# Performance work log

Measured on AMD Instinct MI355X. Metric: run time of the kernel, lower is better.

Reference implementation:

```python
import jax, jax.numpy as jnp
import numpy as np

B, S, H, E, K = 4, 2048, 2048, 8, 2


def setup_inputs() -> dict:
    key = jax.random.key(0)
    k1, k2, k3 = jax.random.split(key, 3)
    scale = 1.0 / np.sqrt(H)
    return {
        "x": jax.random.normal(k1, (B, S, H), dtype=jnp.float32),
        "Wg": jax.random.normal(k2, (H, E), dtype=jnp.float32) * scale,
        "bg": jnp.zeros((E,), dtype=jnp.float32),
        "W": jax.random.normal(k3, (E, H, H), dtype=jnp.float32) * scale,
        "b": jnp.zeros((E, H), dtype=jnp.float32),
        "topk": K,
    }


def reference(x, Wg, bg, W, b, topk):
    Bsz, Sl, Hd = x.shape
    n_exp = W.shape[0]
    hs = x.reshape(-1, Hd)                              # [T, H] flattened tokens
    # Router: linear gate -> softmax -> top-k -> renormalize
    router_logits = hs @ Wg + bg                        # [T, E]
    probs = jax.nn.softmax(router_logits, axis=-1)
    top_w, sel = jax.lax.top_k(probs, topk)             # [T, K]
    top_w = top_w / jnp.sum(top_w, axis=-1, keepdims=True)
    # Per-token combine coefficient for each expert (sums weights over top-k slots)
    coef = jnp.einsum("tk,tke->te", top_w,
                      jax.nn.one_hot(sel, n_exp, dtype=hs.dtype))  # [T, E]
    # Dense grouped expert MLP: y_e = hs @ W_e + b_e, then weighted combine.
    h = jnp.einsum("th,ehf->etf", hs, W) + b[:, None, :]  # [E, T, H]
    out = jnp.einsum("te,etf->tf", coef, h)               # [T, H]
    return out.reshape(Bsz, Sl, Hd), router_logits
```

## Files before the change

### kernel.cpp

```cpp
#include <hip/hip_runtime.h>
#include <math.h>

#define T_TOK 8192
#define HD    2048
#define NE    8
#define BM    128
#define BN    128
#define NT    (HD / 64)
#define MAXT  136
#define RMAX  17408

typedef __bf16 bf16x4 __attribute__((ext_vector_type(4)));
typedef __bf16 bf16x8 __attribute__((ext_vector_type(8)));
typedef float  f32x4  __attribute__((ext_vector_type(4)));

#define GLOAD16(src, dst)                                                              \
    __builtin_amdgcn_global_load_lds((__attribute__((address_space(1))) void*)(src),   \
                                     (__attribute__((address_space(3))) void*)(dst),   \
                                     16, 0, 0)

__global__ __launch_bounds__(256) void router_cvt_kernel(
    const float* __restrict__ x, const float* __restrict__ Wg,
    const float* __restrict__ bg, float* __restrict__ logits_out,
    int* __restrict__ tok_exp, float* __restrict__ tok_w,
    __bf16* __restrict__ xb, int* __restrict__ cnt)
{
    __shared__ int hbin[NE];
    const int lane = threadIdx.x & 63;
    const int wv   = threadIdx.x >> 6;
    const int t    = blockIdx.x * 4 + wv;
    const float* xr  = x  + (size_t)t * HD;
    __bf16*      xbr = xb + (size_t)t * HD;

    if (threadIdx.x < NE) hbin[threadIdx.x] = 0;
    __syncthreads();

    float acc[8] = {0.f,0.f,0.f,0.f,0.f,0.f,0.f,0.f};
#pragma unroll
    for (int j = 0; j < 8; ++j) {
        const int h0 = j * 256 + lane * 4;
        float4 xv = *reinterpret_cast<const float4*>(xr + h0);
        bf16x4 bv;
        bv[0] = (__bf16)xv.x; bv[1] = (__bf16)xv.y;
        bv[2] = (__bf16)xv.z; bv[3] = (__bf16)xv.w;
        *reinterpret_cast<bf16x4*>(xbr + h0) = bv;

        const float4* wg = reinterpret_cast<const float4*>(Wg + (size_t)h0 * NE);
        float xs[4] = {xv.x, xv.y, xv.z, xv.w};
#pragma unroll
        for (int r = 0; r < 4; ++r) {
            float4 wa = wg[r * 2], wb = wg[r * 2 + 1];
            acc[0] += xs[r] * wa.x; acc[1] += xs[r] * wa.y;
            acc[2] += xs[r] * wa.z; acc[3] += xs[r] * wa.w;
            acc[4] += xs[r] * wb.x; acc[5] += xs[r] * wb.y;
            acc[6] += xs[r] * wb.z; acc[7] += xs[r] * wb.w;
        }
    }
#pragma unroll
    for (int off = 32; off; off >>= 1) {
#pragma unroll
        for (int e = 0; e < 8; ++e) acc[e] += __shfl_xor(acc[e], off);
    }
    if (lane == 0) {
        float lg[8];
#pragma unroll
        for (int e = 0; e < 8; ++e) lg[e] = acc[e] + bg[e];
        float4* lo = reinterpret_cast<float4*>(logits_out + (size_t)t * NE);
        lo[0] = make_float4(lg[0], lg[1], lg[2], lg[3]);
        lo[1] = make_float4(lg[4], lg[5], lg[6], lg[7]);
        int i0 = 0;
        for (int e = 1; e < 8; ++e) if (lg[e] > lg[i0]) i0 = e;
        int i1 = (i0 == 0) ? 1 : 0;
        for (int e = 0; e < 8; ++e) if (e != i0 && lg[e] > lg[i1]) i1 = e;
        float d = expf(lg[i1] - lg[i0]);
        float inv = 1.0f / (1.0f + d);
        tok_exp[t * 2]     = i0;
        tok_exp[t * 2 + 1] = i1;
        tok_w[t * 2]       = inv;
        tok_w[t * 2 + 1]   = d * inv;
        atomicAdd(&hbin[i0], 1);
        atomicAdd(&hbin[i1], 1);
    }
    __syncthreads();
    if (threadIdx.x < NE && hbin[threadIdx.x] > 0)
        atomicAdd(&cnt[threadIdx.x], hbin[threadIdx.x]);
}

__global__ __launch_bounds__(256) void wt_kernel(const float* __restrict__ W,
                                                 __bf16* __restrict__ Wt)
{
    const int e  = blockIdx.z;
    const int k0 = blockIdx.y * 64;
    const int f0 = blockIdx.x * 64;
    __shared__ float T[64][65];

    const int t  = threadIdx.x;
    const int fi = (t & 15) * 4;
    const int kb = t >> 4;
    const float* src = W + (size_t)e * HD * HD + (size_t)(k0 + kb) * HD + f0 + fi;
#pragma unroll
    for (int j = 0; j < 4; ++j) {
        float4 v = *reinterpret_cast<const float4*>(src + (size_t)j * 16 * HD);
        int k = kb + j * 16;
        T[k][fi + 0] = v.x;
        T[k][fi + 1] = v.y;
        T[k][fi + 2] = v.z;
        T[k][fi + 3] = v.w;
    }
    __syncthreads();
    const int f  = t >> 2;
    const int kc = (t & 3) * 16;
    bf16x8 o0, o1;
#pragma unroll
    for (int j = 0; j < 8; ++j) o0[j] = (__bf16)T[kc + j][f];
#pragma unroll
    for (int j = 0; j < 8; ++j) o1[j] = (__bf16)T[kc + 8 + j][f];
    __bf16* dst = Wt + (size_t)e * HD * HD + (size_t)(f0 + f) * HD + k0 + kc;
    *reinterpret_cast<bf16x8*>(dst)     = o0;
    *reinterpret_cast<bf16x8*>(dst + 8) = o1;
}

__global__ void scan_kernel(const int* __restrict__ cnt, int* __restrict__ cursor,
                            int* __restrict__ tile_exp, int* __restrict__ tile_row0,
                            int* __restrict__ ntiles)
{
    if (threadIdx.x == 0) {
        int off = 0, nt = 0;
        for (int e = 0; e < NE; ++e) {
            cursor[e] = off;
            int c = cnt[e];
            int tiles = (c + 127) >> 7;
            for (int i = 0; i < tiles; ++i) {
                tile_exp[nt]  = e;
                tile_row0[nt] = off + (i << 7);
                ++nt;
            }
            off += tiles << 7;
        }
        *ntiles = nt;
    }
}

__global__ __launch_bounds__(256) void scatter_kernel(
    const int* __restrict__ tok_exp, const float* __restrict__ tok_w,
    int* __restrict__ cursor, int* __restrict__ row_token, float* __restrict__ row_coef)
{
    __shared__ int lcnt[NE];
    __shared__ int lbase[NE];
    const int tid = threadIdx.x;
    if (tid < NE) lcnt[tid] = 0;
    __syncthreads();
    const int s = blockIdx.x * 256 + tid;
    const int e = tok_exp[s];
    const int r = atomicAdd(&lcnt[e], 1);
    __syncthreads();
    if (tid < NE) lbase[tid] = atomicAdd(&cursor[tid], lcnt[tid]);
    __syncthreads();
    const int pos = lbase[e] + r;
    row_token[pos] = s >> 1;
    row_coef[pos]  = tok_w[s];
}

__global__ __launch_bounds__(256, 2) void moe_gemm_128(
    const __bf16* __restrict__ xb, const __bf16* __restrict__ Wt,
    const float* __restrict__ bexp,
    const int* __restrict__ tile_exp, const int* __restrict__ tile_row0,
    const int* __restrict__ ntiles_p, const int* __restrict__ row_token,
    const float* __restrict__ row_coef, float* __restrict__ out)
{
    const int rt = blockIdx.y;
    if (rt >= *ntiles_p) return;
    const int e  = tile_exp[rt];
    const int r0 = tile_row0[rt];
    const int cb = blockIdx.x * BN;

    __shared__ __align__(16) char lds[65536];

    const int tid  = threadIdx.x;
    const int lane = tid & 63;
    const int wv   = tid >> 6;
    const int wr   = (wv >> 1) * 64;
    const int wc   = (wv & 1) * 64;

    const int colS = ((((tid & 7) * 16) ^ (((tid >> 3) & 7) << 4))) >> 1;

    const __bf16* srcA[4];
    const __bf16* srcB[4];
#pragma unroll
    for (int i = 0; i < 4; ++i) {
        int gr  = i * 32 + (tid >> 3);
        int tok = row_token[r0 + gr];
        if (tok < 0) tok = 0;
        srcA[i] = xb + (size_t)tok * HD + colS;
        srcB[i] = Wt + ((size_t)e << 22) + (size_t)(cb + gr) * HD + colS;
    }

    f32x4 acc[4][4];
#pragma unroll
    for (int m = 0; m < 4; ++m)
#pragma unroll
        for (int n = 0; n < 4; ++n) acc[m][n] = (f32x4){0.f, 0.f, 0.f, 0.f};

    const int fr    = lane & 15;
    const int swz   = (lane & 7) << 4;
    const int koff0 = (((lane >> 4) * 16)      ) ^ swz;
    const int koff1 = (((lane >> 4) * 16) + 64 ) ^ swz;

    {
        char* d0 = lds + wv * 1024;
        char* d1 = d0 + 32768;
#pragma unroll
        for (int i = 0; i < 4; ++i) GLOAD16(srcA[i], d0 + i * 4096);
#pragma unroll
        for (int i = 0; i < 4; ++i) GLOAD16(srcB[i], d0 + 16384 + i * 4096);
#pragma unroll
        for (int i = 0; i < 4; ++i) GLOAD16(srcA[i] + 64, d1 + i * 4096);
#pragma unroll
        for (int i = 0; i < 4; ++i) GLOAD16(srcB[i] + 64, d1 + 16384 + i * 4096);
    }

#pragma unroll 2
    for (int t = 0; t < NT; ++t) {
        if (t < NT - 1) { asm volatile("s_waitcnt vmcnt(8)" ::: "memory"); }
        else            { asm volatile("s_waitcnt vmcnt(0)" ::: "memory"); }
        __builtin_amdgcn_s_barrier();

        const char* ab = lds + (t & 1) * 32768;
        const char* bb = ab + 16384;

        bf16x8 bfr0[4], bfr1[4];
#pragma unroll
        for (int n = 0; n < 4; ++n) {
            int rowb = (wc + n * 16 + fr) << 7;
            bfr0[n] = *reinterpret_cast<const bf16x8*>(bb + (rowb + koff0));
            bfr1[n] = *reinterpret_cast<const bf16x8*>(bb + (rowb + koff1));
        }
        __builtin_amdgcn_s_setprio(1);
#pragma unroll
        for (int m = 0; m < 4; ++m) {
            int rowa = (wr + m * 16 + fr) << 7;
            bf16x8 a0 = *reinterpret_cast<const bf16x8*>(ab + (rowa + koff0));
            bf16x8 a1 = *reinterpret_cast<const bf16x8*>(ab + (rowa + koff1));
#pragma unroll
            for (int n = 0; n < 4; ++n) {
                acc[m][n] = __builtin_amdgcn_mfma_f32_16x16x32_bf16(a0, bfr0[n], acc[m][n], 0, 0, 0);
                acc[m][n] = __builtin_amdgcn_mfma_f32_16x16x32_bf16(a1, bfr1[n], acc[m][n], 0, 0, 0);
            }
        }
        __builtin_amdgcn_s_setprio(0);

        if (t < NT - 2) {
            asm volatile("s_waitcnt lgkmcnt(0)" ::: "memory");
            __builtin_amdgcn_s_barrier();
            const int nk = (t + 2) * 64;
            char* dA = lds + (t & 1) * 32768 + wv * 1024;
#pragma unroll
            for (int i = 0; i < 4; ++i) GLOAD16(srcA[i] + nk, dA + i * 4096);
#pragma unroll
            for (int i = 0; i < 4; ++i) GLOAD16(srcB[i] + nk, dA + 16384 + i * 4096);
        }
    }

    const int rj = (lane >> 4) * 4;
    float bias_[4];
#pragma unroll
    for (int n = 0; n < 4; ++n)
        bias_[n] = bexp[(size_t)e * HD + cb + wc + n * 16 + fr];

#pragma unroll
    for (int m = 0; m < 4; ++m) {
        const int lr = wr + m * 16 + rj;
        int tok[4]; float cf[4];
#pragma unroll
        for (int j = 0; j < 4; ++j) {
            tok[j] = row_token[r0 + lr + j];
            cf[j]  = row_coef[r0 + lr + j];
        }
#pragma unroll
        for (int n = 0; n < 4; ++n) {
            const int f = cb + wc + n * 16 + fr;
#pragma unroll
            for (int j = 0; j < 4; ++j) {
                if (tok[j] >= 0)
                    atomicAdd(&out[(size_t)tok[j] * HD + f], (acc[m][n][j] + bias_[n]) * cf[j]);
            }
        }
    }
}

extern "C" void kernel_launch(void* const* d_in, const int* in_sizes, int n_in,
                              void* d_out, int out_size, void* d_ws, size_t ws_size,
                              hipStream_t stream)
{
    (void)in_sizes; (void)n_in; (void)out_size; (void)ws_size;

    const float* x  = (const float*)d_in[0];
    const float* Wg = (const float*)d_in[1];
    const float* bg = (const float*)d_in[2];
    const float* W  = (const float*)d_in[3];
    const float* b  = (const float*)d_in[4];

    float* out    = (float*)d_out;
    float* logits = out + (size_t)T_TOK * HD;

    char* p = (char*)d_ws;
    int*   cnt       = (int*)p;   p += NE * 4;
    int*   cursor    = (int*)p;   p += NE * 4;
    int*   ntiles    = (int*)p;   p += 8;
    int*   tile_exp  = (int*)p;   p += MAXT * 4;
    int*   tile_row0 = (int*)p;   p += MAXT * 4;
    int*   tok_exp   = (int*)p;   p += T_TOK * 2 * 4;
    float* tok_w     = (float*)p; p += T_TOK * 2 * 4;
    int*   row_token = (int*)p;   p += RMAX * 4;
    float* row_coef  = (float*)p; p += RMAX * 4;
    p = (char*)(((size_t)p + 255) & ~(size_t)255);
    __bf16* xb = (__bf16*)p;      p += (size_t)T_TOK * HD * 2;
    __bf16* Wt = (__bf16*)p;      p += (size_t)NE * HD * HD * 2;

    hipMemsetAsync(cnt, 0, NE * 4, stream);
    hipMemsetAsync(row_token, 0xFF, RMAX * 4, stream);
    hipMemsetAsync(out, 0, (size_t)T_TOK * HD * sizeof(float), stream);

    router_cvt_kernel<<<T_TOK / 4, 256, 0, stream>>>(x, Wg, bg, logits,
                                                     tok_exp, tok_w, xb, cnt);
    wt_kernel<<<dim3(HD / 64, HD / 64, NE), 256, 0, stream>>>(W, Wt);
    scan_kernel<<<1, 64, 0, stream>>>(cnt, cursor, tile_exp, tile_row0, ntiles);
    scatter_kernel<<<T_TOK * 2 / 256, 256, 0, stream>>>(tok_exp, tok_w, cursor,
                                                        row_token, row_coef);

    dim3 grid(HD / BN, MAXT);
    moe_gemm_128<<<grid, 256, 0, stream>>>(xb, Wt, b, tile_exp, tile_row0, ntiles,
                                           row_token, row_coef, out);
}
```

Before: 334.2 us.

## Halve GEMM K-tile to 32 to cut LDS and target four blocks per CU

Shrinks the per-stage K slice of the grouped expert GEMM from 64 to 32. This halves LDS use to 32 KB and raises launch bounds to 4 blocks per CU, with a new swizzled LDS layout that packs two rows per 128-byte line. The aim is more occupancy to hide global-load latency. The cost is twice as many barriers and waitcnt steps per K, and tighter register limits that could cause spills with 64 accumulators per thread.

```diff
diff --git a/kernel.cpp b/kernel.cpp
--- a/kernel.cpp
+++ b/kernel.cpp
@@ -6,7 +6,7 @@
 #define NE    8
 #define BM    128
 #define BN    128
-#define NT    (HD / 64)
+#define NT2   (HD / 32)
 #define MAXT  136
 #define RMAX  17408
 
@@ -161,7 +161,7 @@
     row_coef[pos]  = tok_w[s];
 }
 
-__global__ __launch_bounds__(256, 2) void moe_gemm_128(
+__global__ __launch_bounds__(256, 4) void moe_gemm_128(
     const __bf16* __restrict__ xb, const __bf16* __restrict__ Wt,
     const float* __restrict__ bexp,
     const int* __restrict__ tile_exp, const int* __restrict__ tile_row0,
@@ -174,7 +174,7 @@
     const int r0 = tile_row0[rt];
     const int cb = blockIdx.x * BN;
 
-    __shared__ __align__(16) char lds[65536];
+    __shared__ __align__(16) char lds[32768];
 
     const int tid  = threadIdx.x;
     const int lane = tid & 63;
@@ -182,17 +182,19 @@
     const int wr   = (wv >> 1) * 64;
     const int wc   = (wv & 1) * 64;
 
-    const int colS = ((((tid & 7) * 16) ^ (((tid >> 3) & 7) << 4))) >> 1;
-
-    const __bf16* srcA[4];
-    const __bf16* srcB[4];
-#pragma unroll
-    for (int i = 0; i < 4; ++i) {
-        int gr  = i * 32 + (tid >> 3);
+    const int c2      = (tid & 7) ^ ((tid >> 3) & 7);
+    const int kcolS   = (c2 & 3) * 8;
+    const int rowbase = ((tid >> 3) << 1) + (c2 >> 2);
+
+    const __bf16* srcA[2];
+    const __bf16* srcB[2];
+#pragma unroll
+    for (int i = 0; i < 2; ++i) {
+        int gr  = i * 64 + rowbase;
         int tok = row_token[r0 + gr];
         if (tok < 0) tok = 0;
-        srcA[i] = xb + (size_t)tok * HD + colS;
-        srcB[i] = Wt + ((size_t)e << 22) + (size_t)(cb + gr) * HD + colS;
+        srcA[i] = xb + (size_t)tok * HD + kcolS;
+        srcB[i] = Wt + ((size_t)e << 22) + (size_t)(cb + gr) * HD + kcolS;
     }
 
     f32x4 acc[4][4];
@@ -201,63 +203,59 @@
 #pragma unroll
         for (int n = 0; n < 4; ++n) acc[m][n] = (f32x4){0.f, 0.f, 0.f, 0.f};
 
-    const int fr    = lane & 15;
-    const int swz   = (lane & 7) << 4;
-    const int koff0 = (((lane >> 4) * 16)      ) ^ swz;
-    const int koff1 = (((lane >> 4) * 16) + 64 ) ^ swz;
+    const int fr = lane & 15;
+    const int kb = lane >> 4;
+
+    auto lds_off = [&](int row) -> int {
+        int r2 = row >> 1;
+        return r2 * 128 + (((((row & 1) << 2) + kb) ^ (r2 & 7)) << 4);
+    };
 
     {
         char* d0 = lds + wv * 1024;
-        char* d1 = d0 + 32768;
-#pragma unroll
-        for (int i = 0; i < 4; ++i) GLOAD16(srcA[i], d0 + i * 4096);
-#pragma unroll
-        for (int i = 0; i < 4; ++i) GLOAD16(srcB[i], d0 + 16384 + i * 4096);
-#pragma unroll
-        for (int i = 0; i < 4; ++i) GLOAD16(srcA[i] + 64, d1 + i * 4096);
-#pragma unroll
-        for (int i = 0; i < 4; ++i) GLOAD16(srcB[i] + 64, d1 + 16384 + i * 4096);
+        char* d1 = d0 + 16384;
+#pragma unroll
+        for (int i = 0; i < 2; ++i) GLOAD16(srcA[i],      d0 + i * 4096);
+#pragma unroll
+        for (int i = 0; i < 2; ++i) GLOAD16(srcB[i],      d0 + 8192 + i * 4096);
+#pragma unroll
+        for (int i = 0; i < 2; ++i) GLOAD16(srcA[i] + 32, d1 + i * 4096);
+#pragma unroll
+        for (int i = 0; i < 2; ++i) GLOAD16(srcB[i] + 32, d1 + 8192 + i * 4096);
     }
 
 #pragma unroll 2
-    for (int t = 0; t < NT; ++t) {
-        if (t < NT - 1) { asm volatile("s_waitcnt vmcnt(8)" ::: "memory"); }
-        else            { asm volatile("s_waitcnt vmcnt(0)" ::: "memory"); }
+    for (int t = 0; t < NT2; ++t) {
+        if (t < NT2 - 1) { asm volatile("s_waitcnt vmcnt(4)" ::: "memory"); }
+        else             { asm volatile("s_waitcnt vmcnt(0)" ::: "memory"); }
         __builtin_amdgcn_s_barrier();
 
-        const char* ab = lds + (t & 1) * 32768;
-        const char* bb = ab + 16384;
-
-        bf16x8 bfr0[4], bfr1[4];
-#pragma unroll
-        for (int n = 0; n < 4; ++n) {
-            int rowb = (wc + n * 16 + fr) << 7;
-            bfr0[n] = *reinterpret_cast<const bf16x8*>(bb + (rowb + koff0));
-            bfr1[n] = *reinterpret_cast<const bf16x8*>(bb + (rowb + koff1));
-        }
+        const char* ab = lds + (t & 1) * 16384;
+        const char* bb = ab + 8192;
+
+        bf16x8 bfr[4];
+#pragma unroll
+        for (int n = 0; n < 4; ++n)
+            bfr[n] = *reinterpret_cast<const bf16x8*>(bb + lds_off(wc + n * 16 + fr));
         __builtin_amdgcn_s_setprio(1);
 #pragma unroll
         for (int m = 0; m < 4; ++m) {
-            int rowa = (wr + m * 16 + fr) << 7;
-            bf16x8 a0 = *reinterpret_cast<const bf16x8*>(ab + (rowa + koff0));
-            bf16x8 a1 = *reinterpret_cast<const bf16x8*>(ab + (rowa + koff1));
-#pragma unroll
-            for (int n = 0; n < 4; ++n) {
-                acc[m][n] = __builtin_amdgcn_mfma_f32_16x16x32_bf16(a0, bfr0[n], acc[m][n], 0, 0, 0);
-                acc[m][n] = __builtin_amdgcn_mfma_f32_16x16x32_bf16(a1, bfr1[n], acc[m][n], 0, 0, 0);
-            }
+            bf16x8 a0 = *reinterpret_cast<const bf16x8*>(ab + lds_off(wr + m * 16 + fr));
+#pragma unroll
+            for (int n = 0; n < 4; ++n)
+                acc[m][n] = __builtin_amdgcn_mfma_f32_16x16x32_bf16(a0, bfr[n], acc[m][n], 0, 0, 0);
         }
         __builtin_amdgcn_s_setprio(0);
 
-        if (t < NT - 2) {
+        if (t < NT2 - 2) {
             asm volatile("s_waitcnt lgkmcnt(0)" ::: "memory");
             __builtin_amdgcn_s_barrier();
-            const int nk = (t + 2) * 64;
-            char* dA = lds + (t & 1) * 32768 + wv * 1024;
-#pragma unroll
-            for (int i = 0; i < 4; ++i) GLOAD16(srcA[i] + nk, dA + i * 4096);
-#pragma unroll
-            for (int i = 0; i < 4; ++i) GLOAD16(srcB[i] + nk, dA + 16384 + i * 4096);
+            const int nk = (t + 2) * 32;
+            char* dA = lds + (t & 1) * 16384 + wv * 1024;
+#pragma unroll
+            for (int i = 0; i < 2; ++i) GLOAD16(srcA[i] + nk, dA + i * 4096);
+#pragma unroll
+            for (int i = 0; i < 2; ++i) GLOAD16(srcB[i] + nk, dA + 8192 + i * 4096);
         }
     }
 
```

New measurement: 367.7 us. 10.0% more time.

## Pre-pack expert weights in MFMA fragment order and load B directly to registers

Applied to the files above, without the earlier changes.

The weight transpose kernel now writes each expert matrix in a layout where each lane's MFMA B fragment is a contiguous 16-byte chunk. The GEMM loads B straight from global memory into double-buffered registers instead of staging it through LDS. This halves the LDS footprint so the launch bound asks for three blocks per CU. The trade is more vector registers, and each B fragment is now read from global/L2 by every wave that uses it instead of once per block through shared memory.

```diff
diff --git a/kernel.cpp b/kernel.cpp
--- a/kernel.cpp
+++ b/kernel.cpp
@@ -18,6 +18,8 @@
     __builtin_amdgcn_global_load_lds((__attribute__((address_space(1))) void*)(src),   \
                                      (__attribute__((address_space(3))) void*)(dst),   \
                                      16, 0, 0)
+
+#define MEMFENCE() asm volatile("" ::: "memory")
 
 __global__ __launch_bounds__(256) void router_cvt_kernel(
     const float* __restrict__ x, const float* __restrict__ Wg,
@@ -86,8 +88,8 @@
         atomicAdd(&cnt[threadIdx.x], hbin[threadIdx.x]);
 }
 
-__global__ __launch_bounds__(256) void wt_kernel(const float* __restrict__ W,
-                                                 __bf16* __restrict__ Wt)
+__global__ __launch_bounds__(256) void wt2_kernel(const float* __restrict__ W,
+                                                  __bf16* __restrict__ Wt2)
 {
     const int e  = blockIdx.z;
     const int k0 = blockIdx.y * 64;
@@ -109,15 +111,24 @@
     }
     __syncthreads();
     const int f  = t >> 2;
-    const int kc = (t & 3) * 16;
+    const int c0 = (t & 3) * 2;
+    const int kc = c0 * 8;
     bf16x8 o0, o1;
 #pragma unroll
     for (int j = 0; j < 8; ++j) o0[j] = (__bf16)T[kc + j][f];
 #pragma unroll
     for (int j = 0; j < 8; ++j) o1[j] = (__bf16)T[kc + 8 + j][f];
-    __bf16* dst = Wt + (size_t)e * HD * HD + (size_t)(f0 + f) * HD + k0 + kc;
-    *reinterpret_cast<bf16x8*>(dst)     = o0;
-    *reinterpret_cast<bf16x8*>(dst + 8) = o1;
+
+    const int fb = (f0 >> 4) + (f >> 4);
+#pragma unroll
+    for (int j = 0; j < 2; ++j) {
+        const int ch   = c0 + j;
+        const int kbo  = (k0 >> 5) + (ch >> 2);
+        const int lane = (f & 15) + ((ch & 3) << 4);
+        size_t off = ((size_t)e << 22) + ((size_t)fb << 15) + ((size_t)kbo << 9)
+                   + ((size_t)lane << 3);
+        *reinterpret_cast<bf16x8*>(Wt2 + off) = (j == 0) ? o0 : o1;
+    }
 }
 
 __global__ void scan_kernel(const int* __restrict__ cnt, int* __restrict__ cursor,
@@ -161,8 +172,8 @@
     row_coef[pos]  = tok_w[s];
 }
 
-__global__ __launch_bounds__(256, 2) void moe_gemm_128(
-    const __bf16* __restrict__ xb, const __bf16* __restrict__ Wt,
+__global__ __launch_bounds__(256, 3) void moe_gemm_128(
+    const __bf16* __restrict__ xb, const __bf16* __restrict__ Wt2,
     const float* __restrict__ bexp,
     const int* __restrict__ tile_exp, const int* __restrict__ tile_row0,
     const int* __restrict__ ntiles_p, const int* __restrict__ row_token,
@@ -174,7 +185,7 @@
     const int r0 = tile_row0[rt];
     const int cb = blockIdx.x * BN;
 
-    __shared__ __align__(16) char lds[65536];
+    __shared__ __align__(16) char lds[32768];
 
     const int tid  = threadIdx.x;
     const int lane = tid & 63;
@@ -185,15 +196,16 @@
     const int colS = ((((tid & 7) * 16) ^ (((tid >> 3) & 7) << 4))) >> 1;
 
     const __bf16* srcA[4];
-    const __bf16* srcB[4];
 #pragma unroll
     for (int i = 0; i < 4; ++i) {
         int gr  = i * 32 + (tid >> 3);
         int tok = row_token[r0 + gr];
         if (tok < 0) tok = 0;
         srcA[i] = xb + (size_t)tok * HD + colS;
-        srcB[i] = Wt + ((size_t)e << 22) + (size_t)(cb + gr) * HD + colS;
-    }
+    }
+
+    const __bf16* bptr = Wt2 + ((size_t)e << 22)
+                       + ((size_t)((cb + wc) >> 4) << 15) + ((size_t)lane << 3);
 
     f32x4 acc[4][4];
 #pragma unroll
@@ -206,60 +218,77 @@
     const int koff0 = (((lane >> 4) * 16)      ) ^ swz;
     const int koff1 = (((lane >> 4) * 16) + 64 ) ^ swz;
 
+    bf16x8 breg[2][4][2];
+
     {
         char* d0 = lds + wv * 1024;
-        char* d1 = d0 + 32768;
+        char* d1 = d0 + 16384;
 #pragma unroll
         for (int i = 0; i < 4; ++i) GLOAD16(srcA[i], d0 + i * 4096);
-#pragma unroll
-        for (int i = 0; i < 4; ++i) GLOAD16(srcB[i], d0 + 16384 + i * 4096);
+        MEMFENCE();
+#pragma unroll
+        for (int n = 0; n < 4; ++n)
+#pragma unroll
+            for (int ks = 0; ks < 2; ++ks)
+                breg[0][n][ks] = *reinterpret_cast<const bf16x8*>(
+                    bptr + ((size_t)n << 15) + ((size_t)ks << 9));
+        MEMFENCE();
 #pragma unroll
         for (int i = 0; i < 4; ++i) GLOAD16(srcA[i] + 64, d1 + i * 4096);
-#pragma unroll
-        for (int i = 0; i < 4; ++i) GLOAD16(srcB[i] + 64, d1 + 16384 + i * 4096);
-    }
-
-#pragma unroll 2
-    for (int t = 0; t < NT; ++t) {
-        if (t < NT - 1) { asm volatile("s_waitcnt vmcnt(8)" ::: "memory"); }
-        else            { asm volatile("s_waitcnt vmcnt(0)" ::: "memory"); }
-        __builtin_amdgcn_s_barrier();
-
-        const char* ab = lds + (t & 1) * 32768;
-        const char* bb = ab + 16384;
-
-        bf16x8 bfr0[4], bfr1[4];
-#pragma unroll
-        for (int n = 0; n < 4; ++n) {
-            int rowb = (wc + n * 16 + fr) << 7;
-            bfr0[n] = *reinterpret_cast<const bf16x8*>(bb + (rowb + koff0));
-            bfr1[n] = *reinterpret_cast<const bf16x8*>(bb + (rowb + koff1));
-        }
-        __builtin_amdgcn_s_setprio(1);
-#pragma unroll
-        for (int m = 0; m < 4; ++m) {
-            int rowa = (wr + m * 16 + fr) << 7;
-            bf16x8 a0 = *reinterpret_cast<const bf16x8*>(ab + (rowa + koff0));
-            bf16x8 a1 = *reinterpret_cast<const bf16x8*>(ab + (rowa + koff1));
-#pragma unroll
-            for (int n = 0; n < 4; ++n) {
-                acc[m][n] = __builtin_amdgcn_mfma_f32_16x16x32_bf16(a0, bfr0[n], acc[m][n], 0, 0, 0);
-                acc[m][n] = __builtin_amdgcn_mfma_f32_16x16x32_bf16(a1, bfr1[n], acc[m][n], 0, 0, 0);
-            }
-        }
-        __builtin_amdgcn_s_setprio(0);
-
-        if (t < NT - 2) {
-            asm volatile("s_waitcnt lgkmcnt(0)" ::: "memory");
-            __builtin_amdgcn_s_barrier();
-            const int nk = (t + 2) * 64;
-            char* dA = lds + (t & 1) * 32768 + wv * 1024;
-#pragma unroll
-            for (int i = 0; i < 4; ++i) GLOAD16(srcA[i] + nk, dA + i * 4096);
-#pragma unroll
-            for (int i = 0; i < 4; ++i) GLOAD16(srcB[i] + nk, dA + 16384 + i * 4096);
-        }
-    }
+        MEMFENCE();
+    }
+
+#define K_STEP(T, P)                                                                    \
+    {                                                                                   \
+        if ((T) < NT - 1) { asm volatile("s_waitcnt vmcnt(4)" ::: "memory"); }          \
+        else              { asm volatile("s_waitcnt vmcnt(0)" ::: "memory"); }          \
+        __builtin_amdgcn_s_barrier();                                                   \
+        const char* ab = lds + (P) * 16384;                                             \
+        __builtin_amdgcn_s_setprio(1);                                                  \
+        _Pragma("unroll")                                                               \
+        for (int m = 0; m < 4; ++m) {                                                   \
+            int rowa = (wr + m * 16 + fr) << 7;                                         \
+            bf16x8 a0 = *reinterpret_cast<const bf16x8*>(ab + (rowa + koff0));          \
+            bf16x8 a1 = *reinterpret_cast<const bf16x8*>(ab + (rowa + koff1));          \
+            _Pragma("unroll")                                                           \
+            for (int n = 0; n < 4; ++n) {                                               \
+                acc[m][n] = __builtin_amdgcn_mfma_f32_16x16x32_bf16(a0, breg[P][n][0], acc[m][n], 0, 0, 0); \
+                acc[m][n] = __builtin_amdgcn_mfma_f32_16x16x32_bf16(a1, breg[P][n][1], acc[m][n], 0, 0, 0); \
+            }                                                                           \
+        }                                                                               \
+        __builtin_amdgcn_s_setprio(0);                                                  \
+        if ((T) < NT - 2) {                                                             \
+            asm volatile("s_waitcnt lgkmcnt(0)" ::: "memory");                          \
+            __builtin_amdgcn_s_barrier();                                               \
+            _Pragma("unroll")                                                           \
+            for (int n = 0; n < 4; ++n)                                                 \
+                _Pragma("unroll")                                                       \
+                for (int ks = 0; ks < 2; ++ks)                                          \
+                    breg[(P) ^ 1][n][ks] = *reinterpret_cast<const bf16x8*>(            \
+                        bptr + ((size_t)n << 15) + ((size_t)(((T) + 1) * 2 + ks) << 9)); \
+            MEMFENCE();                                                                 \
+            const int nk = ((T) + 2) * 64;                                              \
+            char* dA = lds + (P) * 16384 + wv * 1024;                                   \
+            _Pragma("unroll")                                                           \
+            for (int i = 0; i < 4; ++i) GLOAD16(srcA[i] + nk, dA + i * 4096);           \
+            MEMFENCE();                                                                 \
+        } else if ((T) == NT - 2) {                                                     \
+                        \
+            _Pragma("unroll")                                                           \
+            for (int n = 0; n < 4; ++n)                                                 \
+                _Pragma("unroll")                                                       \
+                for (int ks = 0; ks < 2; ++ks)                                          \
+                    breg[(P) ^ 1][n][ks] = *reinterpret_cast<const bf16x8*>(            \
+                        bptr + ((size_t)n << 15) + ((size_t)(((T) + 1) * 2 + ks) << 9)); \
+            MEMFENCE();                                                                 \
+        }                                                                               \
+    }
+
+    for (int t = 0; t < NT; t += 2) {
+        K_STEP(t,     0)
+        K_STEP(t + 1, 1)
+    }
+#undef K_STEP
 
     const int rj = (lane >> 4) * 4;
     float bias_[4];
@@ -314,8 +343,8 @@
     int*   row_token = (int*)p;   p += RMAX * 4;
     float* row_coef  = (float*)p; p += RMAX * 4;
     p = (char*)(((size_t)p + 255) & ~(size_t)255);
-    __bf16* xb = (__bf16*)p;      p += (size_t)T_TOK * HD * 2;
-    __bf16* Wt = (__bf16*)p;      p += (size_t)NE * HD * HD * 2;
+    __bf16* xb  = (__bf16*)p;     p += (size_t)T_TOK * HD * 2;
+    __bf16* Wt2 = (__bf16*)p;     p += (size_t)NE * HD * HD * 2;
 
     hipMemsetAsync(cnt, 0, NE * 4, stream);
     hipMemsetAsync(row_token, 0xFF, RMAX * 4, stream);
@@ -323,12 +352,12 @@
 
     router_cvt_kernel<<<T_TOK / 4, 256, 0, stream>>>(x, Wg, bg, logits,
                                                      tok_exp, tok_w, xb, cnt);
-    wt_kernel<<<dim3(HD / 64, HD / 64, NE), 256, 0, stream>>>(W, Wt);
+    wt2_kernel<<<dim3(HD / 64, HD / 64, NE), 256, 0, stream>>>(W, Wt2);
     scan_kernel<<<1, 64, 0, stream>>>(cnt, cursor, tile_exp, tile_row0, ntiles);
     scatter_kernel<<<T_TOK * 2 / 256, 256, 0, stream>>>(tok_exp, tok_w, cursor,
                                                         row_token, row_coef);
 
     dim3 grid(HD / BN, MAXT);
-    moe_gemm_128<<<grid, 256, 0, stream>>>(xb, Wt, b, tile_exp, tile_row0, ntiles,
+    moe_gemm_128<<<grid, 256, 0, stream>>>(xb, Wt2, b, tile_exp, tile_row0, ntiles,
                                            row_token, row_coef, out);
 }
```

New measurement: 355.1 us. +6.3%, slower.
